# Performance work log

Hardware: AMD Instinct MI355X
Metric: run time of the kernel (lower is better)

## Reference

```python
import jax, jax.numpy as jnp
import numpy as np

D_MODEL = 1024
HIDDEN = 4096
N_EXPERTS = 8
LB_COEF = 0.01
B, N = 2, 2048


def setup_inputs() -> dict:
    key = jax.random.key(0)
    k_x, k_g, k_w1, k_w2 = jax.random.split(key, 4)
    s = 0.02
    return {
        "x": jax.random.normal(k_x, (B, N, D_MODEL), dtype=jnp.float32),
        "gate_w": jax.random.normal(k_g, (N_EXPERTS, D_MODEL), dtype=jnp.float32) * s,
        "w1": jax.random.normal(k_w1, (N_EXPERTS, HIDDEN, D_MODEL), dtype=jnp.float32) * s,  # torch Linear weight [out,in]
        "b1": jnp.zeros((N_EXPERTS, HIDDEN), dtype=jnp.float32),
        "w2": jax.random.normal(k_w2, (N_EXPERTS, D_MODEL, HIDDEN), dtype=jnp.float32) * s,
        "b2": jnp.zeros((N_EXPERTS, D_MODEL), dtype=jnp.float32),
    }


def reference(x, gate_w, w1, b1, w2, b2):
    # gate logits: Linear(d_model, E, bias=False)
    logits = jnp.einsum('bnd,ed->bne', x, gate_w)
    probs = jax.nn.softmax(logits, axis=-1)            # router_prob
    gate_scores = jnp.max(probs, axis=-1)              # top-1 prob [B,N]
    sel = jnp.argmax(probs, axis=-1)                   # selected expert [B,N]

    # load-balance aux loss
    onehot = jax.nn.one_hot(sel, N_EXPERTS, dtype=x.dtype)
    f = onehot.mean(axis=(0, 1))                       # fraction of tokens per expert
    P = probs.mean(axis=(0, 1))                        # mean router prob per expert
    aux_loss = LB_COEF * N_EXPERTS * jnp.sum(f * P)

    # dispatch: loop over fixed small expert count (structurally distinct weights)
    out = jnp.zeros_like(x)
    for e in range(N_EXPERTS):
        h = jax.nn.gelu(jnp.einsum('bnd,hd->bnh', x, w1[e]) + b1[e], approximate=False)
        y = jnp.einsum('bnh,dh->bnd', h, w2[e]) + b2[e]
        out = out + jnp.where((sel == e)[..., None], gate_scores[..., None] * y, jnp.zeros((), x.dtype))
    return out, aux_loss
```

## Files before the change

### kernel.cpp

```cpp
#include <hip/hip_runtime.h>
#include <math.h>

#define T_TOK 4096
#define DM 1024
#define HID 4096
#define NEXP 8

typedef unsigned short u16;
typedef __attribute__((ext_vector_type(8))) short short8;
typedef __attribute__((ext_vector_type(4))) float f32x4;

__device__ __forceinline__ u16 f2bf(float f){
  unsigned u = __float_as_uint(f);
  u += 0x7FFF + ((u >> 16) & 1);
  return (u16)(u >> 16);
}
__device__ __forceinline__ float bf2f(u16 b){
  return __uint_as_float(((unsigned)b) << 16);
}

#define GATE_OFF   0u
#define CNT_OFF    16384u
#define LIST_OFF   16512u
#define PROBS_OFF  147584u
#define XB_OFF     278656u
#define H_OFF      8667264u

__global__ void zero_cnt_kernel(int* cnt){
  if (threadIdx.x < NEXP) cnt[threadIdx.x] = 0;
}

__global__ __launch_bounds__(256) void gate_kernel(
    const float* __restrict__ x, const float* __restrict__ gw,
    float* __restrict__ gateo, int* __restrict__ cnt, int* __restrict__ list,
    float* __restrict__ probs, u16* __restrict__ xb)
{
  int tid = threadIdx.x;
  int lane = tid & 63;
  int w = tid >> 6;
  int t = blockIdx.x * 4 + w;

  const float4* x4 = (const float4*)(x + (size_t)t * DM);
  const float4* g4 = (const float4*)gw;

  float acc[8] = {0,0,0,0,0,0,0,0};
  #pragma unroll
  for (int i = 0; i < 4; i++){
    int p = i * 64 + lane;
    float4 xv = x4[p];
    ushort4 pk;
    pk.x = f2bf(xv.x); pk.y = f2bf(xv.y); pk.z = f2bf(xv.z); pk.w = f2bf(xv.w);
    *(ushort4*)&xb[(size_t)t * DM + (size_t)p * 4] = pk;
    #pragma unroll
    for (int e = 0; e < NEXP; e++){
      float4 gv = g4[e * 256 + p];
      acc[e] += xv.x * gv.x + xv.y * gv.y + xv.z * gv.z + xv.w * gv.w;
    }
  }
  #pragma unroll
  for (int e = 0; e < NEXP; e++){
    #pragma unroll
    for (int off = 32; off; off >>= 1)
      acc[e] += __shfl_xor(acc[e], off);
  }
  if (lane == 0){
    float mx = acc[0];
    #pragma unroll
    for (int e = 1; e < NEXP; e++) mx = fmaxf(mx, acc[e]);
    float p[8]; float s = 0.f;
    #pragma unroll
    for (int e = 0; e < NEXP; e++){ p[e] = expf(acc[e] - mx); s += p[e]; }
    float inv = 1.f / s;
    int be = 0; float bp = p[0];
    #pragma unroll
    for (int e = 1; e < NEXP; e++){ if (p[e] > bp){ bp = p[e]; be = e; } }
    #pragma unroll
    for (int e = 0; e < NEXP; e++) probs[(size_t)t * 8 + e] = p[e] * inv;
    gateo[t] = bp * inv;
    int pos = atomicAdd(&cnt[be], 1);
    list[be * T_TOK + pos] = t;
  }
}

__global__ __launch_bounds__(256) void aux_kernel(
    const float* __restrict__ probs, const int* __restrict__ cnt,
    float* __restrict__ aux_out)
{
  __shared__ float sm[256 * 8];
  int tid = threadIdx.x;
  float s[8] = {0,0,0,0,0,0,0,0};
  for (int i = 0; i < 16; i++){
    int t = i * 256 + tid;
    #pragma unroll
    for (int e = 0; e < 8; e++) s[e] += probs[(size_t)t * 8 + e];
  }
  #pragma unroll
  for (int e = 0; e < 8; e++) sm[tid * 8 + e] = s[e];
  __syncthreads();
  for (int st = 128; st; st >>= 1){
    if (tid < st){
      #pragma unroll
      for (int e = 0; e < 8; e++) sm[tid * 8 + e] += sm[(tid + st) * 8 + e];
    }
    __syncthreads();
  }
  if (tid == 0){
    float a = 0.f;
    #pragma unroll
    for (int e = 0; e < 8; e++){
      float f = (float)cnt[e] / (float)T_TOK;
      float P = sm[e] / (float)T_TOK;
      a += f * P;
    }
    aux_out[0] = 0.01f * (float)NEXP * a;
  }
}

template<int KT, int NTOT, bool PHASE2>
__global__ __launch_bounds__(256, 2) void ffn_gemm(
    const u16*  __restrict__ Aall,
    const float* __restrict__ Ball,
    const float* __restrict__ bias,
    const int*  __restrict__ cnt,
    const int*  __restrict__ list,
    const float* __restrict__ gate,
    u16*  __restrict__ hOut,
    float* __restrict__ yOut)
{
  constexpr int NT = NTOT / 128;
  int bid = blockIdx.x;
  int e  = bid / (32 * NT);
  int r  = bid % (32 * NT);
  int mt = r / NT, nt = r % NT;
  int ne = cnt[e];
  int m0 = mt * 128;
  if (m0 >= ne) return;
  const int*   lst = list + e * T_TOK;
  const float* B   = Ball + (size_t)e * NTOT * KT;
  const float* bi  = bias + (size_t)e * NTOT;
  int n0 = nt * 128;

  __shared__ u16 As[128 * 64];
  __shared__ u16 Bs[128 * 64];

  int tid  = threadIdx.x;
  int lane = tid & 63;
  int w    = tid >> 6;
  int wr = (w >> 1) * 64, wc = (w & 1) * 64;
  int fr = lane & 15, fq = lane >> 4;

  const u16*  aSrc[4]; int dstA[4];
  const float* bSrc[4]; int dstB[4];
  #pragma unroll
  for (int i = 0; i < 4; i++){
    int idx = i * 256 + tid;
    int row = idx >> 3, ch = idx & 7;
    int g = ch ^ (row & 7);
    int mrow = m0 + row; if (mrow > ne - 1) mrow = ne - 1;
    int tok = lst[mrow];
    aSrc[i] = Aall + (size_t)tok * KT + g * 8;
    dstA[i] = row * 64 + ch * 8;
    bSrc[i] = B + (size_t)(n0 + row) * KT + g * 8;
    dstB[i] = row * 64 + ch * 8;
  }

  f32x4 acc[4][4];
  #pragma unroll
  for (int m = 0; m < 4; m++)
    #pragma unroll
    for (int n = 0; n < 4; n++)
      acc[m][n] = (f32x4){0.f, 0.f, 0.f, 0.f};

  for (int ks = 0; ks < KT / 64; ++ks){
    if (ks) __syncthreads();
    int ko = ks * 64;
    #pragma unroll
    for (int i = 0; i < 4; i++){
      *(uint4*)&As[dstA[i]] = *(const uint4*)(aSrc[i] + ko);
    }
    #pragma unroll
    for (int i = 0; i < 4; i++){
      const float4* s = (const float4*)(bSrc[i] + ko);
      float4 f0 = s[0], f1 = s[1];
      uint4 p;
      p.x = (unsigned)f2bf(f0.x) | ((unsigned)f2bf(f0.y) << 16);
      p.y = (unsigned)f2bf(f0.z) | ((unsigned)f2bf(f0.w) << 16);
      p.z = (unsigned)f2bf(f1.x) | ((unsigned)f2bf(f1.y) << 16);
      p.w = (unsigned)f2bf(f1.z) | ((unsigned)f2bf(f1.w) << 16);
      *(uint4*)&Bs[dstB[i]] = p;
    }
    __syncthreads();
    #pragma unroll
    for (int kc = 0; kc < 2; kc++){
      short8 a[4], b[4];
      #pragma unroll
      for (int m = 0; m < 4; m++){
        int row = wr + m * 16 + fr;
        int slot = (kc * 4 + fq) ^ (row & 7);
        a[m] = *(const short8*)&As[row * 64 + slot * 8];
      }
      #pragma unroll
      for (int n = 0; n < 4; n++){
        int row = wc + n * 16 + fr;
        int slot = (kc * 4 + fq) ^ (row & 7);
        b[n] = *(const short8*)&Bs[row * 64 + slot * 8];
      }
      #pragma unroll
      for (int m = 0; m < 4; m++)
        #pragma unroll
        for (int n = 0; n < 4; n++)
          acc[m][n] = __builtin_amdgcn_mfma_f32_16x16x32_bf16(a[m], b[n], acc[m][n], 0, 0, 0);
    }
  }

  #pragma unroll
  for (int n = 0; n < 4; n++){
    int col = n0 + wc + n * 16 + fr;
    float bv = bi[col];
    #pragma unroll
    for (int m = 0; m < 4; m++){
      int rbase = m0 + wr + m * 16 + fq * 4;
      f32x4 v = acc[m][n];
      #pragma unroll
      for (int i = 0; i < 4; i++){
        int mrow = rbase + i;
        if (mrow < ne){
          int tok = lst[mrow];
          float val = v[i] + bv;
          if (PHASE2){
            yOut[(size_t)tok * NTOT + col] = gate[tok] * val;
          } else {
            float gl = 0.5f * val * (1.0f + erff(val * 0.70710678118654752f));
            hOut[(size_t)tok * NTOT + col] = f2bf(gl);
          }
        }
      }
    }
  }
}

extern "C" void kernel_launch(void* const* d_in, const int* in_sizes, int n_in,
                              void* d_out, int out_size, void* d_ws, size_t ws_size,
                              hipStream_t stream) {
  const float* x   = (const float*)d_in[0];
  const float* gw  = (const float*)d_in[1];
  const float* w1  = (const float*)d_in[2];
  const float* b1  = (const float*)d_in[3];
  const float* w2  = (const float*)d_in[4];
  const float* b2  = (const float*)d_in[5];

  char* ws = (char*)d_ws;
  float* gateo = (float*)(ws + GATE_OFF);
  int*   cnt   = (int*)  (ws + CNT_OFF);
  int*   list  = (int*)  (ws + LIST_OFF);
  float* probs = (float*)(ws + PROBS_OFF);
  u16*   xb    = (u16*)  (ws + XB_OFF);
  u16*   h     = (u16*)  (ws + H_OFF);

  float* out = (float*)d_out;
  float* aux = out + (size_t)T_TOK * DM;

  hipLaunchKernelGGL(zero_cnt_kernel, dim3(1), dim3(64), 0, stream, cnt);
  hipLaunchKernelGGL(gate_kernel, dim3(T_TOK / 4), dim3(256), 0, stream,
                     x, gw, gateo, cnt, list, probs, xb);
  hipLaunchKernelGGL(aux_kernel, dim3(1), dim3(256), 0, stream, probs, cnt, aux);
  hipLaunchKernelGGL((ffn_gemm<DM, HID, false>), dim3(NEXP * 32 * (HID / 128)), dim3(256), 0, stream,
                     xb, w1, b1, cnt, list, gateo, h, (float*)nullptr);
  hipLaunchKernelGGL((ffn_gemm<HID, DM, true>), dim3(NEXP * 32 * (DM / 128)), dim3(256), 0, stream,
                     h, w2, b2, cnt, list, gateo, (u16*)nullptr, out);
}
```

Measured before the change: 354.7 us.

## Pre-convert expert weights to bf16 and double-buffer GEMM tiles via direct LDS loads

Adds a conversion kernel that turns w1 and w2 to bf16 in workspace on every call, when the workspace is large enough. The FFN GEMMs then stream bf16 tiles with global_load_lds straight into double-buffered shared memory, so the next k-slice loads while MFMAs run on the current one. This removes the repeated per-tile fp32-to-bf16 conversion and halves weight bytes read inside the GEMMs. In exchange it adds a full read/write pass over both weight tensors each call and drops the LDS XOR swizzle, which may cause bank conflicts. A fallback path with fp32 weights, register prefetch and in-kernel conversion is kept for small workspaces.

Result: slower. 410.9 us (+15.8%).

```diff
diff --git a/kernel.cpp b/kernel.cpp
--- a/kernel.cpp
+++ b/kernel.cpp
@@ -14,9 +14,6 @@
   unsigned u = __float_as_uint(f);
   u += 0x7FFF + ((u >> 16) & 1);
   return (u16)(u >> 16);
-}
-__device__ __forceinline__ float bf2f(u16 b){
-  return __uint_as_float(((unsigned)b) << 16);
 }
 
 #define GATE_OFF   0u
@@ -25,9 +22,30 @@
 #define PROBS_OFF  147584u
 #define XB_OFF     278656u
 #define H_OFF      8667264u
+#define W1B_OFF    42221696u
+#define W2B_OFF    109330560u
+#define WS_NEED_BF 176439424u
+
+__device__ __forceinline__ void glds16(const void* g, void* l){
+  __builtin_amdgcn_global_load_lds((const __attribute__((address_space(1))) void*)g,
+                                   (__attribute__((address_space(3))) void*)l, 16, 0, 0);
+}
 
 __global__ void zero_cnt_kernel(int* cnt){
   if (threadIdx.x < NEXP) cnt[threadIdx.x] = 0;
+}
+
+__global__ __launch_bounds__(256) void cvt_kernel(const float* __restrict__ src,
+                                                  u16* __restrict__ dst){
+  size_t i = (size_t)blockIdx.x * 256 + threadIdx.x;
+  const float4* s = (const float4*)src + i * 2;
+  float4 a = s[0], b = s[1];
+  uint4 p;
+  p.x = (unsigned)f2bf(a.x) | ((unsigned)f2bf(a.y) << 16);
+  p.y = (unsigned)f2bf(a.z) | ((unsigned)f2bf(a.w) << 16);
+  p.z = (unsigned)f2bf(b.x) | ((unsigned)f2bf(b.y) << 16);
+  p.w = (unsigned)f2bf(b.z) | ((unsigned)f2bf(b.w) << 16);
+  ((uint4*)dst)[i] = p;
 }
 
 __global__ __launch_bounds__(256) void gate_kernel(
@@ -116,10 +134,11 @@
   }
 }
 
-template<int KT, int NTOT, bool PHASE2>
+template<int KT, int NTOT, bool PHASE2, bool BBF16>
 __global__ __launch_bounds__(256, 2) void ffn_gemm(
     const u16*  __restrict__ Aall,
-    const float* __restrict__ Ball,
+    const u16*  __restrict__ Bb,
+    const float* __restrict__ Bf,
     const float* __restrict__ bias,
     const int*  __restrict__ cnt,
     const int*  __restrict__ list,
@@ -128,6 +147,7 @@
     float* __restrict__ yOut)
 {
   constexpr int NT = NTOT / 128;
+  constexpr int KS = KT / 64;
   int bid = blockIdx.x;
   int e  = bid / (32 * NT);
   int r  = bid % (32 * NT);
@@ -135,13 +155,11 @@
   int ne = cnt[e];
   int m0 = mt * 128;
   if (m0 >= ne) return;
-  const int*   lst = list + e * T_TOK;
-  const float* B   = Ball + (size_t)e * NTOT * KT;
-  const float* bi  = bias + (size_t)e * NTOT;
+  const int* lst = list + e * T_TOK;
   int n0 = nt * 128;
 
-  __shared__ u16 As[128 * 64];
-  __shared__ u16 Bs[128 * 64];
+  __shared__ u16 As[2][8192];
+  __shared__ u16 Bs[2][8192];
 
   int tid  = threadIdx.x;
   int lane = tid & 63;
@@ -149,19 +167,26 @@
   int wr = (w >> 1) * 64, wc = (w & 1) * 64;
   int fr = lane & 15, fq = lane >> 4;
 
-  const u16*  aSrc[4]; int dstA[4];
-  const float* bSrc[4]; int dstB[4];
+  const u16* aS[4];
+  const u16* bS[4];
   #pragma unroll
   for (int i = 0; i < 4; i++){
-    int idx = i * 256 + tid;
-    int row = idx >> 3, ch = idx & 7;
-    int g = ch ^ (row & 7);
+    int seg = w * 4 + i;
+    int row = seg * 8 + (lane >> 3);
+    int ch  = lane & 7;
     int mrow = m0 + row; if (mrow > ne - 1) mrow = ne - 1;
-    int tok = lst[mrow];
-    aSrc[i] = Aall + (size_t)tok * KT + g * 8;
-    dstA[i] = row * 64 + ch * 8;
-    bSrc[i] = B + (size_t)(n0 + row) * KT + g * 8;
-    dstB[i] = row * 64 + ch * 8;
+    aS[i] = Aall + (size_t)lst[mrow] * KT + ch * 8;
+    if (BBF16) bS[i] = Bb + (size_t)e * NTOT * KT + (size_t)(n0 + row) * KT + ch * 8;
+  }
+  const float* fS[4]; int fD[4];
+  if (!BBF16){
+    #pragma unroll
+    for (int i = 0; i < 4; i++){
+      int idx = i * 256 + tid;
+      int row = idx >> 3, ch = idx & 7;
+      fS[i] = Bf + (size_t)e * NTOT * KT + (size_t)(n0 + row) * KT + ch * 8;
+      fD[i] = row * 64 + ch * 8;
+    }
   }
 
   f32x4 acc[4][4];
@@ -171,52 +196,79 @@
     for (int n = 0; n < 4; n++)
       acc[m][n] = (f32x4){0.f, 0.f, 0.f, 0.f};
 
-  for (int ks = 0; ks < KT / 64; ++ks){
-    if (ks) __syncthreads();
-    int ko = ks * 64;
+  #pragma unroll
+  for (int i = 0; i < 4; i++){
+    int seg = w * 4 + i;
+    glds16(aS[i], &As[0][seg * 512]);
+    if (BBF16) glds16(bS[i], &Bs[0][seg * 512]);
+  }
+  if (!BBF16){
     #pragma unroll
     for (int i = 0; i < 4; i++){
-      *(uint4*)&As[dstA[i]] = *(const uint4*)(aSrc[i] + ko);
-    }
-    #pragma unroll
-    for (int i = 0; i < 4; i++){
-      const float4* s = (const float4*)(bSrc[i] + ko);
-      float4 f0 = s[0], f1 = s[1];
+      float4 f0 = ((const float4*)fS[i])[0], f1 = ((const float4*)fS[i])[1];
       uint4 p;
       p.x = (unsigned)f2bf(f0.x) | ((unsigned)f2bf(f0.y) << 16);
       p.y = (unsigned)f2bf(f0.z) | ((unsigned)f2bf(f0.w) << 16);
       p.z = (unsigned)f2bf(f1.x) | ((unsigned)f2bf(f1.y) << 16);
       p.w = (unsigned)f2bf(f1.z) | ((unsigned)f2bf(f1.w) << 16);
-      *(uint4*)&Bs[dstB[i]] = p;
-    }
-    __syncthreads();
+      *(uint4*)&Bs[0][fD[i]] = p;
+    }
+  }
+  __syncthreads();
+
+  int buf = 0;
+  for (int ks = 0; ks < KS; ++ks){
+    int nxt = ks + 1;
+    float4 pf0[4], pf1[4];
+    if (nxt < KS){
+      if (!BBF16){
+        #pragma unroll
+        for (int i = 0; i < 4; i++){
+          const float4* s = (const float4*)(fS[i] + nxt * 64);
+          pf0[i] = s[0]; pf1[i] = s[1];
+        }
+      }
+      #pragma unroll
+      for (int i = 0; i < 4; i++){
+        int seg = w * 4 + i;
+        glds16(aS[i] + nxt * 64, &As[buf ^ 1][seg * 512]);
+        if (BBF16) glds16(bS[i] + nxt * 64, &Bs[buf ^ 1][seg * 512]);
+      }
+    }
     #pragma unroll
     for (int kc = 0; kc < 2; kc++){
       short8 a[4], b[4];
       #pragma unroll
-      for (int m = 0; m < 4; m++){
-        int row = wr + m * 16 + fr;
-        int slot = (kc * 4 + fq) ^ (row & 7);
-        a[m] = *(const short8*)&As[row * 64 + slot * 8];
-      }
-      #pragma unroll
-      for (int n = 0; n < 4; n++){
-        int row = wc + n * 16 + fr;
-        int slot = (kc * 4 + fq) ^ (row & 7);
-        b[n] = *(const short8*)&Bs[row * 64 + slot * 8];
-      }
+      for (int m = 0; m < 4; m++)
+        a[m] = *(const short8*)&As[buf][(wr + m * 16 + fr) * 64 + (kc * 4 + fq) * 8];
+      #pragma unroll
+      for (int n = 0; n < 4; n++)
+        b[n] = *(const short8*)&Bs[buf][(wc + n * 16 + fr) * 64 + (kc * 4 + fq) * 8];
       #pragma unroll
       for (int m = 0; m < 4; m++)
         #pragma unroll
         for (int n = 0; n < 4; n++)
           acc[m][n] = __builtin_amdgcn_mfma_f32_16x16x32_bf16(a[m], b[n], acc[m][n], 0, 0, 0);
     }
+    if (nxt < KS && !BBF16){
+      #pragma unroll
+      for (int i = 0; i < 4; i++){
+        uint4 p;
+        p.x = (unsigned)f2bf(pf0[i].x) | ((unsigned)f2bf(pf0[i].y) << 16);
+        p.y = (unsigned)f2bf(pf0[i].z) | ((unsigned)f2bf(pf0[i].w) << 16);
+        p.z = (unsigned)f2bf(pf1[i].x) | ((unsigned)f2bf(pf1[i].y) << 16);
+        p.w = (unsigned)f2bf(pf1[i].z) | ((unsigned)f2bf(pf1[i].w) << 16);
+        *(uint4*)&Bs[buf ^ 1][fD[i]] = p;
+      }
+    }
+    __syncthreads();
+    buf ^= 1;
   }
 
   #pragma unroll
   for (int n = 0; n < 4; n++){
     int col = n0 + wc + n * 16 + fr;
-    float bv = bi[col];
+    float bv = bias[(size_t)e * NTOT + col];
     #pragma unroll
     for (int m = 0; m < 4; m++){
       int rbase = m0 + wr + m * 16 + fq * 4;
@@ -256,16 +308,32 @@
   float* probs = (float*)(ws + PROBS_OFF);
   u16*   xb    = (u16*)  (ws + XB_OFF);
   u16*   h     = (u16*)  (ws + H_OFF);
+  u16*   w1b   = (u16*)  (ws + W1B_OFF);
+  u16*   w2b   = (u16*)  (ws + W2B_OFF);
 
   float* out = (float*)d_out;
   float* aux = out + (size_t)T_TOK * DM;
 
+  bool useBF = ws_size >= (size_t)WS_NEED_BF;
+
   hipLaunchKernelGGL(zero_cnt_kernel, dim3(1), dim3(64), 0, stream, cnt);
+  if (useBF){
+    hipLaunchKernelGGL(cvt_kernel, dim3(16384), dim3(256), 0, stream, w1, w1b);
+    hipLaunchKernelGGL(cvt_kernel, dim3(16384), dim3(256), 0, stream, w2, w2b);
+  }
   hipLaunchKernelGGL(gate_kernel, dim3(T_TOK / 4), dim3(256), 0, stream,
                      x, gw, gateo, cnt, list, probs, xb);
   hipLaunchKernelGGL(aux_kernel, dim3(1), dim3(256), 0, stream, probs, cnt, aux);
-  hipLaunchKernelGGL((ffn_gemm<DM, HID, false>), dim3(NEXP * 32 * (HID / 128)), dim3(256), 0, stream,
-                     xb, w1, b1, cnt, list, gateo, h, (float*)nullptr);
-  hipLaunchKernelGGL((ffn_gemm<HID, DM, true>), dim3(NEXP * 32 * (DM / 128)), dim3(256), 0, stream,
-                     h, w2, b2, cnt, list, gateo, (u16*)nullptr, out);
-}
+
+  if (useBF){
+    hipLaunchKernelGGL((ffn_gemm<DM, HID, false, true>), dim3(NEXP * 32 * (HID / 128)), dim3(256), 0, stream,
+                       xb, w1b, (const float*)nullptr, b1, cnt, list, gateo, h, (float*)nullptr);
+    hipLaunchKernelGGL((ffn_gemm<HID, DM, true, true>), dim3(NEXP * 32 * (DM / 128)), dim3(256), 0, stream,
+                       h, w2b, (const float*)nullptr, b2, cnt, list, gateo, (u16*)nullptr, out);
+  } else {
+    hipLaunchKernelGGL((ffn_gemm<DM, HID, false, false>), dim3(NEXP * 32 * (HID / 128)), dim3(256), 0, stream,
+                       xb, (const u16*)nullptr, w1, b1, cnt, list, gateo, h, (float*)nullptr);
+    hipLaunchKernelGGL((ffn_gemm<HID, DM, true, false>), dim3(NEXP * 32 * (DM / 128)), dim3(256), 0, stream,
+                       h, (const u16*)nullptr, w2, b2, cnt, list, gateo, (u16*)nullptr, out);
+  }
+}
```

## Double-buffer expert GEMMs with direct global-to-LDS loads and larger 256-row tiles

Applied to the files above, without the earlier changes.

Rewrites the grouped expert FFN GEMM as a double-buffered pipeline. A tiles are loaded with global_load_lds straight into shared memory. Fp32 weight tiles are prefetched into registers two steps ahead and converted to bf16 into the alternate buffer. Blocks grow to 512 threads covering 256 token rows, and the second GEMM uses 64-wide N tiles. The aim is to hide global load latency and reuse weights across more tokens. The cost is more LDS and registers per block and hand-written waitcnt and barrier sequencing that is fragile.

Result: slower. 377.5 us (+6.4%).

```diff
diff --git a/kernel.cpp b/kernel.cpp
--- a/kernel.cpp
+++ b/kernel.cpp
@@ -14,9 +14,6 @@
   unsigned u = __float_as_uint(f);
   u += 0x7FFF + ((u >> 16) & 1);
   return (u16)(u >> 16);
-}
-__device__ __forceinline__ float bf2f(u16 b){
-  return __uint_as_float(((unsigned)b) << 16);
 }
 
 #define GATE_OFF   0u
@@ -25,6 +22,18 @@
 #define PROBS_OFF  147584u
 #define XB_OFF     278656u
 #define H_OFF      8667264u
+
+__device__ __forceinline__ void glds16(const void* g, void* l){
+  __builtin_amdgcn_global_load_lds((const __attribute__((address_space(1))) void*)g,
+                                   (__attribute__((address_space(3))) void*)l, 16, 0, 0);
+}
+
+#define LGKM0  asm volatile("s_waitcnt lgkmcnt(0)" ::: "memory")
+#define VMW8   asm volatile("s_waitcnt vmcnt(8)" ::: "memory")
+#define VMW6   asm volatile("s_waitcnt vmcnt(6)" ::: "memory")
+#define VMW0   asm volatile("s_waitcnt vmcnt(0)" ::: "memory")
+#define SBAR() __builtin_amdgcn_s_barrier()
+#define SCHED0 __builtin_amdgcn_sched_barrier(0)
 
 __global__ void zero_cnt_kernel(int* cnt){
   if (threadIdx.x < NEXP) cnt[threadIdx.x] = 0;
@@ -116,10 +125,10 @@
   }
 }
 
-template<int KT, int NTOT, bool PHASE2>
-__global__ __launch_bounds__(256, 2) void ffn_gemm(
+template<int BN, int K, int BNTOT, bool PHASE2>
+__global__ __launch_bounds__(512, 2) void ffn_gemm(
     const u16*  __restrict__ Aall,
-    const float* __restrict__ Ball,
+    const float* __restrict__ Bf,
     const float* __restrict__ bias,
     const int*  __restrict__ cnt,
     const int*  __restrict__ list,
@@ -127,99 +136,129 @@
     u16*  __restrict__ hOut,
     float* __restrict__ yOut)
 {
-  constexpr int NT = NTOT / 128;
+  constexpr int NT  = BNTOT / BN;
+  constexpr int KS  = K / 64;
+  constexpr int NFR = BN / 32;
+  constexpr int BLD = BN / 32;
+
   int bid = blockIdx.x;
-  int e  = bid / (32 * NT);
-  int r  = bid % (32 * NT);
-  int mt = r / NT, nt = r % NT;
+  int nt = bid % NT;
+  int r2 = bid / NT;
+  int mt = r2 & 15;
+  int e  = r2 >> 4;
   int ne = cnt[e];
-  int m0 = mt * 128;
+  int m0 = mt * 256;
   if (m0 >= ne) return;
-  const int*   lst = list + e * T_TOK;
-  const float* B   = Ball + (size_t)e * NTOT * KT;
-  const float* bi  = bias + (size_t)e * NTOT;
-  int n0 = nt * 128;
-
-  __shared__ u16 As[128 * 64];
-  __shared__ u16 Bs[128 * 64];
+  const int* lst = list + e * T_TOK;
+  int n0 = nt * BN;
+
+  __shared__ u16 As[2][16384];
+  __shared__ u16 Bs[2][BN * 64];
 
   int tid  = threadIdx.x;
   int lane = tid & 63;
   int w    = tid >> 6;
-  int wr = (w >> 1) * 64, wc = (w & 1) * 64;
+  int wm = w >> 1, wn = w & 1;
   int fr = lane & 15, fq = lane >> 4;
 
-  const u16*  aSrc[4]; int dstA[4];
-  const float* bSrc[4]; int dstB[4];
+  const u16* aS[4];
   #pragma unroll
   for (int i = 0; i < 4; i++){
-    int idx = i * 256 + tid;
-    int row = idx >> 3, ch = idx & 7;
-    int g = ch ^ (row & 7);
-    int mrow = m0 + row; if (mrow > ne - 1) mrow = ne - 1;
-    int tok = lst[mrow];
-    aSrc[i] = Aall + (size_t)tok * KT + g * 8;
-    dstA[i] = row * 64 + ch * 8;
-    bSrc[i] = B + (size_t)(n0 + row) * KT + g * 8;
-    dstB[i] = row * 64 + ch * 8;
-  }
-
-  f32x4 acc[4][4];
+    int seg = w * 4 + i;
+    int r   = seg * 8 + (lane >> 3);
+    int g   = (lane & 7) ^ (r & 7);
+    int mrow = m0 + r; if (mrow > ne - 1) mrow = ne - 1;
+    aS[i] = Aall + (size_t)lst[mrow] * K + g * 8;
+  }
+
+  const float* bS[BLD]; int bwOff[BLD];
+  {
+    int c = tid & 15;
+    #pragma unroll
+    for (int j = 0; j < BLD; j++){
+      int r = (tid >> 4) + j * 32;
+      bS[j] = Bf + ((size_t)e * BNTOT + n0 + r) * K + c * 4;
+      bwOff[j] = r * 64 + (((c >> 1) ^ (r & 7)) * 8) + (c & 1) * 4;
+    }
+  }
+
+  f32x4 acc[4][NFR];
   #pragma unroll
   for (int m = 0; m < 4; m++)
     #pragma unroll
-    for (int n = 0; n < 4; n++)
+    for (int n = 0; n < NFR; n++)
       acc[m][n] = (f32x4){0.f, 0.f, 0.f, 0.f};
 
-  for (int ks = 0; ks < KT / 64; ++ks){
-    if (ks) __syncthreads();
-    int ko = ks * 64;
-    #pragma unroll
-    for (int i = 0; i < 4; i++){
-      *(uint4*)&As[dstA[i]] = *(const uint4*)(aSrc[i] + ko);
-    }
-    #pragma unroll
-    for (int i = 0; i < 4; i++){
-      const float4* s = (const float4*)(bSrc[i] + ko);
-      float4 f0 = s[0], f1 = s[1];
-      uint4 p;
-      p.x = (unsigned)f2bf(f0.x) | ((unsigned)f2bf(f0.y) << 16);
-      p.y = (unsigned)f2bf(f0.z) | ((unsigned)f2bf(f0.w) << 16);
-      p.z = (unsigned)f2bf(f1.x) | ((unsigned)f2bf(f1.y) << 16);
-      p.w = (unsigned)f2bf(f1.z) | ((unsigned)f2bf(f1.w) << 16);
-      *(uint4*)&Bs[dstB[i]] = p;
-    }
-    __syncthreads();
-    #pragma unroll
-    for (int kc = 0; kc < 2; kc++){
-      short8 a[4], b[4];
-      #pragma unroll
-      for (int m = 0; m < 4; m++){
-        int row = wr + m * 16 + fr;
-        int slot = (kc * 4 + fq) ^ (row & 7);
-        a[m] = *(const short8*)&As[row * 64 + slot * 8];
-      }
-      #pragma unroll
-      for (int n = 0; n < 4; n++){
-        int row = wc + n * 16 + fr;
-        int slot = (kc * 4 + fq) ^ (row & 7);
-        b[n] = *(const short8*)&Bs[row * 64 + slot * 8];
-      }
-      #pragma unroll
-      for (int m = 0; m < 4; m++)
-        #pragma unroll
-        for (int n = 0; n < 4; n++)
-          acc[m][n] = __builtin_amdgcn_mfma_f32_16x16x32_bf16(a[m], b[n], acc[m][n], 0, 0, 0);
-    }
-  }
-
-  #pragma unroll
-  for (int n = 0; n < 4; n++){
-    int col = n0 + wc + n * 16 + fr;
-    float bv = bi[col];
+  float4 bregA[BLD], bregB[BLD];
+
+  #pragma unroll
+  for (int j = 0; j < BLD; j++) bregA[j] = *(const float4*)(bS[j]);
+  #pragma unroll
+  for (int i = 0; i < 4; i++){ int seg = w * 4 + i; glds16(aS[i], &As[0][seg * 512]); }
+  #pragma unroll
+  for (int j = 0; j < BLD; j++) bregB[j] = *(const float4*)(bS[j] + 64);
+  #pragma unroll
+  for (int i = 0; i < 4; i++){ int seg = w * 4 + i; glds16(aS[i] + 64, &As[1][seg * 512]); }
+  if (BLD == 4) { VMW8; } else { VMW6; }
+  SCHED0;
+  #pragma unroll
+  for (int j = 0; j < BLD; j++){
+    uint2 pk;
+    pk.x = (unsigned)f2bf(bregA[j].x) | ((unsigned)f2bf(bregA[j].y) << 16);
+    pk.y = (unsigned)f2bf(bregA[j].z) | ((unsigned)f2bf(bregA[j].w) << 16);
+    *(uint2*)&Bs[0][bwOff[j]] = pk;
+  }
+  LGKM0; SBAR();
+
+#define STEP(P, T, BRI, BRW)                                                     \
+  {                                                                              \
+    short8 afr[4][2]; short8 bfr[NFR][2];                                        \
+    _Pragma("unroll") for (int m = 0; m < 4; m++)                                \
+      _Pragma("unroll") for (int kc = 0; kc < 2; kc++){                          \
+        int row = wm * 64 + m * 16 + fr; int slot = (kc * 4 + fq) ^ (row & 7);   \
+        afr[m][kc] = *(const short8*)&As[P][row * 64 + slot * 8]; }              \
+    _Pragma("unroll") for (int n = 0; n < NFR; n++)                              \
+      _Pragma("unroll") for (int kc = 0; kc < 2; kc++){                          \
+        int row = wn * (BN / 2) + n * 16 + fr;                                   \
+        int slot = (kc * 4 + fq) ^ (row & 7);                                    \
+        bfr[n][kc] = *(const short8*)&Bs[P][row * 64 + slot * 8]; }              \
+    LGKM0; SBAR();                                                               \
+    if ((T) + 1 < KS){                                                           \
+      if ((T) + 2 < KS){                                                         \
+        _Pragma("unroll") for (int j = 0; j < BLD; j++)                          \
+          BRI[j] = *(const float4*)(bS[j] + (size_t)((T) + 2) * 64);             \
+        _Pragma("unroll") for (int i = 0; i < 4; i++){ int seg = w * 4 + i;      \
+          glds16(aS[i] + (size_t)((T) + 2) * 64, &As[P][seg * 512]); }           \
+        if (BLD == 4) { VMW8; } else { VMW6; }                                   \
+      } else { VMW0; }                                                           \
+      SCHED0;                                                                    \
+      _Pragma("unroll") for (int j = 0; j < BLD; j++){                           \
+        uint2 pk;                                                                \
+        pk.x = (unsigned)f2bf(BRW[j].x) | ((unsigned)f2bf(BRW[j].y) << 16);      \
+        pk.y = (unsigned)f2bf(BRW[j].z) | ((unsigned)f2bf(BRW[j].w) << 16);      \
+        *(uint2*)&Bs[P ^ 1][bwOff[j]] = pk; }                                    \
+      LGKM0; SBAR();                                                             \
+    }                                                                            \
+    _Pragma("unroll") for (int m = 0; m < 4; m++)                                \
+      _Pragma("unroll") for (int n = 0; n < NFR; n++){                           \
+        acc[m][n] = __builtin_amdgcn_mfma_f32_16x16x32_bf16(afr[m][0], bfr[n][0], acc[m][n], 0, 0, 0); \
+        acc[m][n] = __builtin_amdgcn_mfma_f32_16x16x32_bf16(afr[m][1], bfr[n][1], acc[m][n], 0, 0, 0); \
+      }                                                                          \
+  }
+
+  for (int t = 0; t < KS; t += 2){
+    STEP(0, t,     bregA, bregB)
+    STEP(1, t + 1, bregB, bregA)
+  }
+#undef STEP
+
+  #pragma unroll
+  for (int n = 0; n < NFR; n++){
+    int col = n0 + wn * (BN / 2) + n * 16 + fr;
+    float bv = bias[(size_t)e * BNTOT + col];
     #pragma unroll
     for (int m = 0; m < 4; m++){
-      int rbase = m0 + wr + m * 16 + fq * 4;
+      int rbase = m0 + wm * 64 + m * 16 + fq * 4;
       f32x4 v = acc[m][n];
       #pragma unroll
       for (int i = 0; i < 4; i++){
@@ -228,10 +267,10 @@
           int tok = lst[mrow];
           float val = v[i] + bv;
           if (PHASE2){
-            yOut[(size_t)tok * NTOT + col] = gate[tok] * val;
+            yOut[(size_t)tok * DM + col] = gate[tok] * val;
           } else {
             float gl = 0.5f * val * (1.0f + erff(val * 0.70710678118654752f));
-            hOut[(size_t)tok * NTOT + col] = f2bf(gl);
+            hOut[(size_t)tok * HID + col] = f2bf(gl);
           }
         }
       }
@@ -264,8 +303,11 @@
   hipLaunchKernelGGL(gate_kernel, dim3(T_TOK / 4), dim3(256), 0, stream,
                      x, gw, gateo, cnt, list, probs, xb);
   hipLaunchKernelGGL(aux_kernel, dim3(1), dim3(256), 0, stream, probs, cnt, aux);
-  hipLaunchKernelGGL((ffn_gemm<DM, HID, false>), dim3(NEXP * 32 * (HID / 128)), dim3(256), 0, stream,
+
+  hipLaunchKernelGGL((ffn_gemm<128, DM, HID, false>),
+                     dim3(NEXP * 16 * (HID / 128)), dim3(512), 0, stream,
                      xb, w1, b1, cnt, list, gateo, h, (float*)nullptr);
-  hipLaunchKernelGGL((ffn_gemm<HID, DM, true>), dim3(NEXP * 32 * (DM / 128)), dim3(256), 0, stream,
+  hipLaunchKernelGGL((ffn_gemm<64, HID, DM, true>),
+                     dim3(NEXP * 16 * (DM / 64)), dim3(512), 0, stream,
                      h, w2, b2, cnt, list, gateo, (u16*)nullptr, out);
 }
```
